# Kernel tuning notes

Measured on AMD Instinct MI355X. Metric: run time of the kernel, lower is better.

## Reference

```python
import jax, jax.numpy as jnp
import numpy as np

L_COORD = 5.0
L_NOOBJ = 0.5
NUM_CLS = 20


def setup_inputs() -> dict:
    key = jax.random.key(0)
    k1, k2, k3, k4, k5, k6, k7 = jax.random.split(key, 7)
    BS, S, MAXOBJ = 2048, 14, 20
    # post-sigmoid style predictions in [0,1): [conf,x,y,w,h]*2 + 20 classes
    pred = jax.random.uniform(k1, (BS, S, S, 30), jnp.float32)
    # valid GT boxes: x1,y1,x2,y2 in [0,1] with positive w,h; class index stored as float
    x1 = jax.random.uniform(k2, (BS, MAXOBJ)) * 0.75
    y1 = jax.random.uniform(k3, (BS, MAXOBJ)) * 0.75
    w = jax.random.uniform(k4, (BS, MAXOBJ)) * 0.2 + 0.02
    h = jax.random.uniform(k5, (BS, MAXOBJ)) * 0.2 + 0.02
    cls = jax.random.randint(k6, (BS, MAXOBJ), 0, NUM_CLS).astype(jnp.float32)
    target = jnp.stack([x1, y1, x1 + w, y1 + h, cls], axis=-1)
    valid = (jax.random.uniform(k7, (BS, MAXOBJ)) > 0.3).astype(jnp.float32)
    target = target * valid[..., None]
    return {"pred": pred, "target": target}


def build_target(target, pred_boxes, grids):
    """target: (BS,MaxObj,5); pred_boxes: (BS,2,S,S,5) [conf,x,y,w,h].
    Returns confxywh (BS,2,S,S,5) and class one-hots (BS,S,S,20).
    Sequential scan over object slots preserves the torch loop's
    last-write-wins semantics when two objects land in the same cell."""
    bs = target.shape[0]
    bidx = jnp.arange(bs)
    conf0 = jnp.zeros((bs, 2, grids, grids, 5), pred_boxes.dtype)
    clc0 = jnp.zeros((bs, grids, grids, NUM_CLS), pred_boxes.dtype)
    fg = float(grids)

    def step(carry, obj):  # obj: (BS,5)
        conf, clc = carry
        x1, y1, x2, y2, cls = (obj[:, i] for i in range(5))
        valid = obj.sum(axis=1) != 0
        cx = (x1 + x2) * 0.5 * fg
        cy = (y1 + y2) * 0.5 * fg
        w = x2 - x1
        h = y2 - y1
        gx = jnp.clip(jnp.floor(cx).astype(jnp.int32), 0, grids - 1)
        gy = jnp.clip(jnp.floor(cy).astype(jnp.int32), 0, grids - 1)
        offx = cx - gx
        offy = cy - gy
        # responsible-cell predictions: (BS,2,5) -> xywh
        pb = pred_boxes[bidx, :, gy, gx]
        pxy = pb[..., 1:3] / fg
        pwh = pb[..., 3:5]
        p_lt = pxy - 0.5 * pwh
        p_rb = pxy + 0.5 * pwh
        t_ctr = jnp.stack([offx, offy], -1) / fg  # matches original (uses offsets, not cx/cy)
        t_wh = jnp.stack([w, h], -1)
        t_lt = t_ctr - 0.5 * t_wh
        t_rb = t_ctr + 0.5 * t_wh
        lt = jnp.maximum(p_lt, t_lt[:, None, :])
        rb = jnp.minimum(p_rb, t_rb[:, None, :])
        whi = jnp.clip(rb - lt, 0.0, None)
        inter = whi[..., 0] * whi[..., 1]
        a1 = (p_rb[..., 0] - p_lt[..., 0]) * (p_rb[..., 1] - p_lt[..., 1])
        a2 = ((t_rb[..., 0] - t_lt[..., 0]) * (t_rb[..., 1] - t_lt[..., 1]))[:, None]
        iou = inter / (a1 + a2 - inter)  # (BS,2)
        mi = jnp.argmax(iou, axis=1).astype(jnp.int32)
        # invalid rows: redirect to an out-of-range grid row, dropped by scatter
        gy_s = jnp.where(valid, gy, grids)
        vals = jnp.stack([jnp.ones_like(offx), offx, offy, w, h], -1)
        conf = conf.at[bidx, mi, gy_s, gx].set(vals, mode="drop")
        clc = clc.at[bidx, gy_s, gx, cls.astype(jnp.int32)].set(1.0, mode="drop")
        return (conf, clc), None

    (conf, clc), _ = jax.lax.scan(step, (conf0, clc0), jnp.swapaxes(target, 0, 1))
    return conf, clc


def _yolo_loss(pred, target):
    bs, S = pred.shape[0], pred.shape[2]
    pred_b = pred[..., :10].reshape(bs, S, S, 2, 5).transpose(0, 3, 1, 2, 4)  # (BS,2,S,S,5)
    pred_cls = pred[..., 10:]  # (BS,S,S,20)
    conf, clc = build_target(target, pred_b, S)

    conf_sum = conf[:, 0, :, :, 0] + conf[:, 1, :, :, 0]  # (BS,S,S)
    obj_m = conf_sum == 1.0
    noobj_m = conf_sum == 0.0
    noobj_m2 = jnp.broadcast_to(noobj_m[:, None], (bs, 2, S, S))

    n_noobj = jnp.sum(noobj_m2.astype(pred.dtype))
    noobj_loss = jnp.sum(noobj_m2 * (pred_b[..., 0] - conf[..., 0]) ** 2) / n_noobj

    # responsible box rows = obj cells AND non-zero target row (selectMask in torch)
    resp = obj_m[:, None] & (jnp.sum(conf, axis=-1) != 0)  # (BS,2,S,S)
    resp_f = resp.astype(pred.dtype)
    n_resp = jnp.sum(resp_f)

    objconf_loss = jnp.sum(resp_f * (pred_b[..., 0] - conf[..., 0]) ** 2) / n_resp
    loss_xy = jnp.sum(resp_f[..., None] * (pred_b[..., 1:3] - conf[..., 1:3]) ** 2) / (n_resp * 2.0)

    # safe sqrt: masked-out entries replaced by 1.0 to keep grads finite
    rm = resp[..., None]
    p_wh = jnp.sqrt(jnp.where(rm, pred_b[..., 3:5], 1.0))
    t_wh = jnp.sqrt(jnp.where(rm, conf[..., 3:5], 1.0))
    loss_wh = jnp.sum(resp_f[..., None] * (p_wh - t_wh) ** 2) / (n_resp * 2.0)

    obj_f = obj_m.astype(pred.dtype)
    n_obj = jnp.sum(obj_f)
    loss_clc = jnp.sum(obj_f[..., None] * (pred_cls - clc) ** 2) / (n_obj * NUM_CLS)

    return L_COORD * (loss_xy + loss_wh) + objconf_loss + L_NOOBJ * noobj_loss + loss_clc


def reference(pred, target):
    return _yolo_loss(pred, target)
```

## Files before the change

### kernel.cpp

```cpp
#include <hip/hip_runtime.h>
#include <math.h>

#define NBATCH 2048
#define GS 14
#define NCELL (GS * GS)
#define NCH 30
#define NPRED (NCELL * NCH)
#define NQ (NPRED / 4)
#define NQ2 (2 * NQ)
#define MAXOBJ 20
#define NCLS 20
#define THREADS 256
#define BLOCKS 1024

typedef float v4f __attribute__((ext_vector_type(4)));


__global__ __launch_bounds__(256) void yolo_main_kernel(
        const float* __restrict__ pred,
        const float* __restrict__ target,
        float* __restrict__ ws)
{
    __shared__ float s_red[4][8];
    const int blk = blockIdx.x;
    const int b0 = blk * 2;
    const int tid = threadIdx.x;
    const int wave = tid >> 6;
    const int lane = tid & 63;
    const float fg = (float)GS;
    const int b = b0 + wave;

    v4f xr[12];
    {
        const v4f* g4 = (const v4f*)(pred + (size_t)b0 * NPRED);
        #pragma unroll
        for (int k = 0; k < 12; ++k) {
            int i = tid + k * THREADS;
            int ic = (i < NQ2) ? i : (NQ2 - 1);
            xr[k] = __builtin_nontemporal_load(&g4[ic]);
        }
    }

    float t0 = 0.f, t1 = 0.f, t2 = 0.f, t3 = 0.f, t4 = 0.f;
    if (wave < 2 && lane < MAXOBJ) {
        const float* tb = target + (size_t)b * (MAXOBJ * 5) + lane * 5;
        t0 = tb[0]; t1 = tb[1]; t2 = tb[2]; t3 = tb[3]; t4 = tb[4];
    }

    float acc = 0.f;
    #pragma unroll
    for (int k = 0; k < 12; ++k) {
        int i = tid + k * THREADS;
        if (i < NQ2) {
            v4f x = xr[k];
            int r = (4 * i) % NCH;
            if (r == 0 || r == 5)  acc += x[0] * x[0];
            if (r == 4 || r == 29) acc += x[1] * x[1];
            if (r == 3 || r == 28) acc += x[2] * x[2];
            if (r == 2 || r == 27) acc += x[3] * x[3];
        }
    }

    float v0 = 0.f, v1 = 0.f, v2 = 0.f, v3 = 0.f, v4 = 0.f, v5 = 0.f, v6 = 0.f;
    if (wave < 2) {
        const int o = lane;
        bool valid = false;
        int cell = 0, mi = 0, cls = 0;
        float offx = 0.f, offy = 0.f, w = 0.f, h = 0.f;
        float pc[10];
        #pragma unroll
        for (int i = 0; i < 10; ++i) pc[i] = 0.f;

        if (o < MAXOBJ && (t0 + t1 + t2 + t3 + t4) != 0.0f) {
            valid = true;
            float cx = (t0 + t2) * 0.5f * fg;
            float cy = (t1 + t3) * 0.5f * fg;
            w = t2 - t0;
            h = t3 - t1;
            int gx = min(max((int)floorf(cx), 0), GS - 1);
            int gy = min(max((int)floorf(cy), 0), GS - 1);
            offx = cx - (float)gx;
            offy = cy - (float)gy;
            cell = gy * GS + gx;
            cls = (int)t4;
            const float2* p2 = (const float2*)(pred + ((size_t)b * NCELL + cell) * NCH);
            #pragma unroll
            for (int i = 0; i < 5; ++i) {
                float2 xx = p2[i];
                pc[2 * i] = xx.x;
                pc[2 * i + 1] = xx.y;
            }
            float tcx = offx / fg, tcy = offy / fg;
            float tlx = tcx - 0.5f * w, tly = tcy - 0.5f * h;
            float trx = tcx + 0.5f * w, trY = tcy + 0.5f * h;
            float ta = (trx - tlx) * (trY - tly);
            float iou0, iou1;
            {
                float px = pc[1] / fg, py = pc[2] / fg;
                float pw = pc[3], ph = pc[4];
                float plx = px - 0.5f * pw, ply = py - 0.5f * ph;
                float prx = px + 0.5f * pw, prY = py + 0.5f * ph;
                float ix = fmaxf(fminf(prx, trx) - fmaxf(plx, tlx), 0.f);
                float iy = fmaxf(fminf(prY, trY) - fmaxf(ply, tly), 0.f);
                float inter = ix * iy;
                float a1 = (prx - plx) * (prY - ply);
                iou0 = inter / (a1 + ta - inter);
            }
            {
                float px = pc[6] / fg, py = pc[7] / fg;
                float pw = pc[8], ph = pc[9];
                float plx = px - 0.5f * pw, ply = py - 0.5f * ph;
                float prx = px + 0.5f * pw, prY = py + 0.5f * ph;
                float ix = fmaxf(fminf(prx, trx) - fmaxf(plx, tlx), 0.f);
                float iy = fmaxf(fminf(prY, trY) - fmaxf(ply, tly), 0.f);
                float inter = ix * iy;
                float a1 = (prx - plx) * (prY - ply);
                iou1 = inter / (a1 + ta - inter);
            }
            mi = (iou1 > iou0) ? 1 : 0;
        }

        int pack = cell | (mi << 8) | (cls << 16);
        unsigned long long vm = __ballot(valid);

        bool win = valid;
        #pragma unroll
        for (int j = 0; j < MAXOBJ; ++j) {
            int pj = __shfl(pack, j);
            if (((vm >> j) & 1ull) && j > o && (pj & 0x1FF) == (pack & 0x1FF))
                win = false;
        }
        unsigned long long wm = __ballot(win);

        bool other = false;
        bool rep = win;
        unsigned int clsmask = 0u;
        #pragma unroll
        for (int j = 0; j < MAXOBJ; ++j) {
            int pj = __shfl(pack, j);
            int cj = pj & 0xFF;
            int mj = (pj >> 8) & 1;
            int clj = (pj >> 16) & 0xFF;
            bool vj = (vm >> j) & 1ull;
            bool wj = (wm >> j) & 1ull;
            if (wj && cj == cell && mj != mi) other = true;
            if (wj && j < o && cj == cell) rep = false;
            if (vj && cj == cell) clsmask |= (1u << clj);
        }

        if (rep) {
            v0 = pc[0] * pc[0] + pc[5] * pc[5];
            v1 = 1.0f;
        }
        if (win && !other) {
            float conf = mi ? pc[5] : pc[0];
            float px   = mi ? pc[6] : pc[1];
            float py   = mi ? pc[7] : pc[2];
            float pw   = mi ? pc[8] : pc[3];
            float ph   = mi ? pc[9] : pc[4];
            float dconf = conf - 1.0f;
            v2 = dconf * dconf;
            float dx = px - offx, dy = py - offy;
            v3 = dx * dx + dy * dy;
            float sw = sqrtf(pw) - sqrtf(w);
            float sh = sqrtf(ph) - sqrtf(h);
            v4 = sw * sw + sh * sh;
            const float2* p2 = (const float2*)(pred + ((size_t)b * NCELL + cell) * NCH);
            float clc = 0.f;
            #pragma unroll
            for (int k = 0; k < 10; ++k) {
                float2 xx = p2[5 + k];
                float c0 = ((clsmask >> (2 * k)) & 1u) ? 1.0f : 0.0f;
                float c1 = ((clsmask >> (2 * k + 1)) & 1u) ? 1.0f : 0.0f;
                float d0 = xx.x - c0, d1 = xx.y - c1;
                clc += d0 * d0 + d1 * d1;
            }
            v5 = clc;
            v6 = 1.0f;
        }

        #pragma unroll
        for (int off = 32; off > 0; off >>= 1) {
            v0 += __shfl_down(v0, off);
            v1 += __shfl_down(v1, off);
            v2 += __shfl_down(v2, off);
            v3 += __shfl_down(v3, off);
            v4 += __shfl_down(v4, off);
            v5 += __shfl_down(v5, off);
            v6 += __shfl_down(v6, off);
        }
    }

    #pragma unroll
    for (int off = 32; off > 0; off >>= 1) acc += __shfl_down(acc, off);

    if (lane == 0) {
        s_red[wave][7] = acc;
        if (wave < 2) {
            s_red[wave][0] = v0; s_red[wave][1] = v1; s_red[wave][2] = v2;
            s_red[wave][3] = v3; s_red[wave][4] = v4; s_red[wave][5] = v5;
            s_red[wave][6] = v6;
        }
    }
    __syncthreads();
    if (tid == 0) {
        float* p = ws + (size_t)blk * 8;
        #pragma unroll
        for (int k = 0; k < 7; ++k) p[k] = s_red[0][k] + s_red[1][k];
        p[7] = s_red[0][7] + s_red[1][7] + s_red[2][7] + s_red[3][7];
    }
}

__global__ __launch_bounds__(256) void yolo_final_kernel(
        const float* __restrict__ ws,
        float* __restrict__ out)
{
    __shared__ float s_red[4][8];
    const int tid = threadIdx.x;
    const int wave = tid >> 6;
    const int lane = tid & 63;

    float v[8] = {0.f, 0.f, 0.f, 0.f, 0.f, 0.f, 0.f, 0.f};
    for (int r = tid; r < BLOCKS; r += THREADS) {
        const float4* p = (const float4*)(ws + (size_t)r * 8);
        float4 x0 = p[0];
        float4 x1 = p[1];
        v[0] += x0.x; v[1] += x0.y; v[2] += x0.z; v[3] += x0.w;
        v[4] += x1.x; v[5] += x1.y; v[6] += x1.z; v[7] += x1.w;
    }
    #pragma unroll
    for (int off = 32; off > 0; off >>= 1) {
        #pragma unroll
        for (int k = 0; k < 8; ++k) v[k] += __shfl_down(v[k], off);
    }
    if (lane == 0) {
        #pragma unroll
        for (int k = 0; k < 8; ++k) s_red[wave][k] = v[k];
    }
    __syncthreads();
    if (tid == 0) {
        float s_sub     = s_red[0][0] + s_red[1][0] + s_red[2][0] + s_red[3][0];
        float c_occ     = s_red[0][1] + s_red[1][1] + s_red[2][1] + s_red[3][1];
        float s_objconf = s_red[0][2] + s_red[1][2] + s_red[2][2] + s_red[3][2];
        float s_xy      = s_red[0][3] + s_red[1][3] + s_red[2][3] + s_red[3][3];
        float s_wh      = s_red[0][4] + s_red[1][4] + s_red[2][4] + s_red[3][4];
        float s_clc     = s_red[0][5] + s_red[1][5] + s_red[2][5] + s_red[3][5];
        float c_obj1    = s_red[0][6] + s_red[1][6] + s_red[2][6] + s_red[3][6];
        float s_all     = s_red[0][7] + s_red[1][7] + s_red[2][7] + s_red[3][7];

        float s_noobj = s_all - s_sub;
        float c_noobj = (float)(NBATCH * NCELL) - c_occ;
        float n_noobj = 2.0f * c_noobj;
        float n_resp  = c_obj1;
        float noobj_loss   = s_noobj / n_noobj;
        float objconf_loss = s_objconf / n_resp;
        float loss_xy  = s_xy / (n_resp * 2.0f);
        float loss_wh  = s_wh / (n_resp * 2.0f);
        float loss_clc = s_clc / (c_obj1 * (float)NCLS);
        out[0] = 5.0f * (loss_xy + loss_wh) + objconf_loss
               + 0.5f * noobj_loss + loss_clc;
    }
}

extern "C" void kernel_launch(void* const* d_in, const int* in_sizes, int n_in,
                              void* d_out, int out_size, void* d_ws, size_t ws_size,
                              hipStream_t stream) {
    const float* pred = (const float*)d_in[0];
    const float* target = (const float*)d_in[1];
    float* ws = (float*)d_ws;
    float* out = (float*)d_out;

    yolo_main_kernel<<<BLOCKS, THREADS, 0, stream>>>(pred, target, ws);
    yolo_final_kernel<<<1, THREADS, 0, stream>>>(ws, out);
}
```

Before: 17.92 us.

## Load only confidence-channel quads instead of full prediction tensor; four batches per block

The noobj sum now reads only the 16-byte quads that hold the two confidence channels of each cell, through a global work index, instead of streaming every prediction float. Block count is halved and each of the four waves handles one batch's object matching, so no wave sits idle. This targets HBM traffic, since most of the tensor was loaded only to be masked off, but the scattered 16-byte gathers may use DRAM bursts less efficiently.

```diff
diff --git a/kernel.cpp b/kernel.cpp
--- a/kernel.cpp
+++ b/kernel.cpp
@@ -6,12 +6,15 @@
 #define NCELL (GS * GS)
 #define NCH 30
 #define NPRED (NCELL * NCH)
-#define NQ (NPRED / 4)
-#define NQ2 (2 * NQ)
 #define MAXOBJ 20
 #define NCLS 20
 #define THREADS 256
-#define BLOCKS 1024
+#define BLOCKS 512
+
+#define NWIN 200704
+#define NWORK (NWIN * 4)
+#define TOT_THREADS (BLOCKS * THREADS)
+#define NITER 7
 
 typedef float v4f __attribute__((ext_vector_type(4)));
 
@@ -23,46 +26,48 @@
 {
     __shared__ float s_red[4][8];
     const int blk = blockIdx.x;
-    const int b0 = blk * 2;
     const int tid = threadIdx.x;
     const int wave = tid >> 6;
     const int lane = tid & 63;
     const float fg = (float)GS;
-    const int b = b0 + wave;
-
-    v4f xr[12];
+    const int b = blk * 4 + wave;
+    const int gtid = blk * THREADS + tid;
+
+    v4f xr[NITER];
+    int wm_[NITER];
     {
-        const v4f* g4 = (const v4f*)(pred + (size_t)b0 * NPRED);
-        #pragma unroll
-        for (int k = 0; k < 12; ++k) {
-            int i = tid + k * THREADS;
-            int ic = (i < NQ2) ? i : (NQ2 - 1);
-            xr[k] = __builtin_nontemporal_load(&g4[ic]);
+        const v4f* g4 = (const v4f*)pred;
+        #pragma unroll
+        for (int k = 0; k < NITER; ++k) {
+            int w = gtid + k * TOT_THREADS;
+            int wc = (w < NWORK) ? w : (NWORK - 1);
+            int g = wc >> 2;
+            int m = wc & 3;
+            int q = g * 15 + (m & 1) + ((m >> 1) * 7);
+            wm_[k] = (w < NWORK) ? m : -1;
+            xr[k] = __builtin_nontemporal_load(&g4[q]);
         }
     }
 
     float t0 = 0.f, t1 = 0.f, t2 = 0.f, t3 = 0.f, t4 = 0.f;
-    if (wave < 2 && lane < MAXOBJ) {
+    if (lane < MAXOBJ) {
         const float* tb = target + (size_t)b * (MAXOBJ * 5) + lane * 5;
         t0 = tb[0]; t1 = tb[1]; t2 = tb[2]; t3 = tb[3]; t4 = tb[4];
     }
 
     float acc = 0.f;
     #pragma unroll
-    for (int k = 0; k < 12; ++k) {
-        int i = tid + k * THREADS;
-        if (i < NQ2) {
+    for (int k = 0; k < NITER; ++k) {
+        int m = wm_[k];
+        if (m >= 0) {
             v4f x = xr[k];
-            int r = (4 * i) % NCH;
-            if (r == 0 || r == 5)  acc += x[0] * x[0];
-            if (r == 4 || r == 29) acc += x[1] * x[1];
-            if (r == 3 || r == 28) acc += x[2] * x[2];
-            if (r == 2 || r == 27) acc += x[3] * x[3];
+            float val = (m == 0) ? x[0] : (m == 1) ? x[1] : (m == 2) ? x[2] : x[3];
+            acc += val * val;
         }
     }
 
     float v0 = 0.f, v1 = 0.f, v2 = 0.f, v3 = 0.f, v4 = 0.f, v5 = 0.f, v6 = 0.f;
-    if (wave < 2) {
+    {
         const int o = lane;
         bool valid = false;
         int cell = 0, mi = 0, cls = 0;
@@ -130,7 +135,7 @@
             if (((vm >> j) & 1ull) && j > o && (pj & 0x1FF) == (pack & 0x1FF))
                 win = false;
         }
-        unsigned long long wm = __ballot(win);
+        unsigned long long wmask = __ballot(win);
 
         bool other = false;
         bool rep = win;
@@ -142,7 +147,7 @@
             int mj = (pj >> 8) & 1;
             int clj = (pj >> 16) & 0xFF;
             bool vj = (vm >> j) & 1ull;
-            bool wj = (wm >> j) & 1ull;
+            bool wj = (wmask >> j) & 1ull;
             if (wj && cj == cell && mj != mi) other = true;
             if (wj && j < o && cj == cell) rep = false;
             if (vj && cj == cell) clsmask |= (1u << clj);
@@ -195,19 +200,16 @@
     for (int off = 32; off > 0; off >>= 1) acc += __shfl_down(acc, off);
 
     if (lane == 0) {
-        s_red[wave][7] = acc;
-        if (wave < 2) {
-            s_red[wave][0] = v0; s_red[wave][1] = v1; s_red[wave][2] = v2;
-            s_red[wave][3] = v3; s_red[wave][4] = v4; s_red[wave][5] = v5;
-            s_red[wave][6] = v6;
-        }
+        s_red[wave][0] = v0; s_red[wave][1] = v1; s_red[wave][2] = v2;
+        s_red[wave][3] = v3; s_red[wave][4] = v4; s_red[wave][5] = v5;
+        s_red[wave][6] = v6; s_red[wave][7] = acc;
     }
     __syncthreads();
     if (tid == 0) {
         float* p = ws + (size_t)blk * 8;
         #pragma unroll
-        for (int k = 0; k < 7; ++k) p[k] = s_red[0][k] + s_red[1][k];
-        p[7] = s_red[0][7] + s_red[1][7] + s_red[2][7] + s_red[3][7];
+        for (int k = 0; k < 8; ++k)
+            p[k] = s_red[0][k] + s_red[1][k] + s_red[2][k] + s_red[3][k];
     }
 }
 
```

New measurement: 17.53 us. -2.2%, faster.
